# Kernel tuning notes

Measured on AMD Instinct MI355X. Metric: run time of the kernel, lower is better.

## Reference

```python
import jax, jax.numpy as jnp
import numpy as np

B, T, C, H, NUM_EDGE_TYPES = 2, 512, 256, 8, 16


def setup_inputs() -> dict:
    key = jax.random.key(0)
    ks = jax.random.split(key, 8)
    init = 0.02
    x = jax.random.normal(ks[0], (B, T, C), dtype=jnp.float32)
    bias_matrix = jax.random.randint(ks[1], (B, T, T), 0, NUM_EDGE_TYPES)
    w_attn = jax.random.normal(ks[2], (C, 3 * C), dtype=jnp.float32) * init
    w_proj = jax.random.normal(ks[3], (C, C), dtype=jnp.float32) * init
    w_edge_k = jax.random.normal(ks[4], (C, C), dtype=jnp.float32) * init
    w_edge_v = jax.random.normal(ks[5], (C, C), dtype=jnp.float32) * init
    edge_emb_table = jax.random.normal(ks[6], (NUM_EDGE_TYPES, C), dtype=jnp.float32)
    attn_bias_table = jax.random.normal(ks[7], (NUM_EDGE_TYPES, H), dtype=jnp.float32)
    return {
        "x": x,
        "bias_matrix": bias_matrix,
        "w_attn": w_attn,
        "w_proj": w_proj,
        "w_edge_k": w_edge_k,
        "w_edge_v": w_edge_v,
        "edge_emb_table": edge_emb_table,
        "attn_bias_table": attn_bias_table,
    }


def reference(x, bias_matrix, w_attn, w_proj, w_edge_k, w_edge_v,
              edge_emb_table, attn_bias_table):
    b, t, c = x.shape
    h = attn_bias_table.shape[1]
    e = c // h
    scale = jnp.sqrt(jnp.asarray(e, x.dtype))

    qkv = x @ w_attn                              # (B,T,3C)
    q, k, v = jnp.split(qkv, 3, axis=-1)
    # (B,H,T,E)
    q = q.reshape(b, t, h, e).transpose(0, 2, 1, 3)
    k = k.reshape(b, t, h, e).transpose(0, 2, 1, 3)
    v = v.reshape(b, t, h, e).transpose(0, 2, 1, 3)

    # edge-type embeddings and per-pair k/v modulation, (B,T,T,H,E)
    ee = edge_emb_table[bias_matrix]              # (B,T,T,C)
    e_k = (ee @ w_edge_k).reshape(b, t, t, h, e)
    e_v = (ee @ w_edge_v).reshape(b, t, t, h, e)

    # scores[b,h,i,j] = sum_e q[b,h,i,e] * k[b,h,j,e] * e_k[b, j, i, h, e]
    # (torch: e_k permuted to (B,H,j,i,E), broadcast-multiplied by k then
    #  contracted with q via 'bhie,bhjie->bhij')
    scores = jnp.einsum('bhie,bhje,bjihe->bhij', q, k, e_k) / scale

    causal = jnp.tril(jnp.ones((t, t), dtype=bool))  # (T,T)
    scores = jnp.where(causal, scores, -jnp.inf)

    # edge-type attention bias: (B,T,T,H) -> (B,H,T,T), zeroed above diagonal
    bias = attn_bias_table[bias_matrix].transpose(0, 3, 1, 2)
    bias = jnp.where(causal, bias, jnp.zeros((), bias.dtype))

    attn = jax.nn.softmax(scores + bias, axis=-1)  # (B,H,T,T)

    # y[b,h,i,e] = sum_j attn[b,h,i,j] * v[b,h,j,e] * e_v[b, j, i, h, e]
    y = jnp.einsum('bhij,bhje,bjihe->bhie', attn, v, e_v)
    y = y.transpose(0, 2, 1, 3).reshape(b, t, c)
    return y @ w_proj
```

## Files before the change

kernel.cpp:

```cpp
#include <hip/hip_runtime.h>
#include <hip/hip_bf16.h>
#include <math.h>

#define Bdim 2
#define Tdim 512
#define Cdim 256
#define Hdim 8
#define Edim 32
#define NTYPES 16
#define TI 8
#define JT 128

__global__ __launch_bounds__(256) void pre_kernel(
    const float* __restrict__ A, const float* __restrict__ Bw,
    const float* __restrict__ emb, const float* __restrict__ wk,
    const float* __restrict__ wv,
    float* __restrict__ qT, float* __restrict__ kT, float* __restrict__ vT,
    float* __restrict__ ekt, float* __restrict__ evt)
{
    __shared__ float smem[16 * 34 + 16 * 64];
    int tid = threadIdx.x;

    if (blockIdx.x >= 384) {
        int t = blockIdx.x - 384;
        float* se = smem;
        se[tid] = emb[t * Cdim + tid];
        __syncthreads();
        float a = 0.f, b = 0.f;
        for (int k = 0; k < Cdim; ++k) {
            float ev = se[k];
            a = fmaf(ev, wk[k * Cdim + tid], a);
            b = fmaf(ev, wv[k * Cdim + tid], b);
        }
        ekt[t * Cdim + tid] = a;
        evt[t * Cdim + tid] = b;
        return;
    }

    const int N = 3 * Cdim;
    const int K = Cdim;
    float (*As)[34] = (float(*)[34])smem;
    float (*Bs)[64] = (float(*)[64])(smem + 16 * 34);
    int m0 = (blockIdx.x / 12) * 32;
    int n0 = (blockIdx.x % 12) * 64;
    int tr = tid >> 4, tc = tid & 15;
    float acc[2][4] = {};
    int bkr = tid >> 4, bcq = (tid & 15) * 4;

    for (int k0 = 0; k0 < K; k0 += 16) {
        if (tid < 128) {
            int r = tid >> 2, kq = (tid & 3) * 4;
            float4 av = *(const float4*)(A + (size_t)(m0 + r) * K + k0 + kq);
            As[kq + 0][r] = av.x;
            As[kq + 1][r] = av.y;
            As[kq + 2][r] = av.z;
            As[kq + 3][r] = av.w;
        }
        float4 bv = *(const float4*)(Bw + (size_t)(k0 + bkr) * N + n0 + bcq);
        *(float4*)&Bs[bkr][bcq] = bv;
        __syncthreads();
#pragma unroll
        for (int kk = 0; kk < 16; ++kk) {
            float2 a2 = *(float2*)&As[kk][tr * 2];
            float4 b4 = *(float4*)&Bs[kk][tc * 4];
            acc[0][0] = fmaf(a2.x, b4.x, acc[0][0]);
            acc[0][1] = fmaf(a2.x, b4.y, acc[0][1]);
            acc[0][2] = fmaf(a2.x, b4.z, acc[0][2]);
            acc[0][3] = fmaf(a2.x, b4.w, acc[0][3]);
            acc[1][0] = fmaf(a2.y, b4.x, acc[1][0]);
            acc[1][1] = fmaf(a2.y, b4.y, acc[1][1]);
            acc[1][2] = fmaf(a2.y, b4.z, acc[1][2]);
            acc[1][3] = fmaf(a2.y, b4.w, acc[1][3]);
        }
        __syncthreads();
    }
    int sec = n0 >> 8;
    float* dst = (sec == 0) ? qT : (sec == 1) ? kT : vT;
    int cc0 = (n0 & 255) + tc * 4;
    int h = cc0 >> 5;
    int e0 = cc0 & 31;
#pragma unroll
    for (int i = 0; i < 2; ++i) {
        int m = m0 + tr * 2 + i;
        int bq = m >> 9, t = m & (Tdim - 1);
        float4 val = make_float4(acc[i][0], acc[i][1], acc[i][2], acc[i][3]);
        *(float4*)&dst[(((size_t)bq * Hdim + h) * Tdim + t) * Edim + e0] = val;
    }
}

__global__ __launch_bounds__(512, 4) void attn_kernel(
    const float* __restrict__ qT, const float* __restrict__ kT,
    const float* __restrict__ vT, const int* __restrict__ bm,
    const float* __restrict__ ekt, const float* __restrict__ evt,
    const float* __restrict__ abt, float* __restrict__ y)
{
    __shared__ float qm[TI][NTYPES][32];
    __shared__ float ss[TI][512];
    __shared__ unsigned int st1pf[Tdim];
    __shared__ float sevt[NTYPES][36];
    __shared__ float sabt[NTYPES];
    __shared__ float sinv[TI];

    float* spart = (float*)ss;

    const int tau = 63 - (blockIdx.x >> 4);
    const int bh = blockIdx.x & 15;
    const int h = bh & (Hdim - 1);
    const int b = bh >> 3;
    const int tid = threadIdx.x;
    const int wave = tid >> 6;
    const int lane = tid & 63;
    const float inv_scale = 0.17677669529663687f;

    const float* qbase = qT + (size_t)bh * Tdim * Edim;
    const float* kbase = kT + (size_t)bh * Tdim * Edim;
    const float* vbase = vT + (size_t)bh * Tdim * Edim;
    const int* bmb = bm + (size_t)b * Tdim * Tdim;

    const int i0 = tau * TI;
    const int imax = i0 + TI - 1;
    const int njt = (imax >> 7) + 1;
    const int jmax = njt << 7;

    if (tid < 128) {
        int t = tid >> 3, eq = tid & 7;
        *(float4*)&sevt[t][eq * 4] = *(const float4*)&evt[t * Cdim + h * Edim + eq * 4];
    }
    if (tid < NTYPES) sabt[tid] = abt[tid * Hdim + h];
    if (tid < jmax) {
        const int* rowp = bmb + (size_t)tid * Tdim + i0;
        int4 lo = *(const int4*)rowp;
        int4 hi = *(const int4*)(rowp + 4);
        st1pf[tid] =
            ((unsigned)(lo.x & 15)) | (((unsigned)(lo.y & 15)) << 4) |
            (((unsigned)(lo.z & 15)) << 8) | (((unsigned)(lo.w & 15)) << 12) |
            (((unsigned)(hi.x & 15)) << 16) | (((unsigned)(hi.y & 15)) << 20) |
            (((unsigned)(hi.z & 15)) << 24) | (((unsigned)(hi.w & 15)) << 28);
    }
    for (int idx = tid; idx < TI * NTYPES * 8; idx += 512) {
        int eq = idx & 7;
        int t = (idx >> 3) & (NTYPES - 1);
        int r = idx >> 7;
        float4 qv = *(const float4*)&qbase[(size_t)(i0 + r) * Edim + eq * 4];
        float4 ev = *(const float4*)&ekt[t * Cdim + h * Edim + eq * 4];
        float4 o;
        o.x = qv.x * ev.x; o.y = qv.y * ev.y;
        o.z = qv.z * ev.z; o.w = qv.w * ev.w;
        *(float4*)&qm[r][t][(eq << 2) ^ ((t & 7) << 2)] = o;
    }
    __syncthreads();

    {
        const int jsub = wave & 1;
        const int ii0 = wave >> 1;
        const int jl = (jsub << 6) + lane;
        for (int jt = 0; jt < njt; ++jt) {
            int j0 = jt << 7;
            if (j0 + (jsub << 6) > imax) break;
            int j = j0 + jl;
            unsigned tp = st1pf[j];
            const float* krow = kbase + ((size_t)j << 5);
            float4 k4[8];
#pragma unroll
            for (int eq = 0; eq < 8; ++eq)
                k4[eq] = *(const float4*)(krow + eq * 4);

#pragma unroll
            for (int u = 0; u < 2; ++u) {
                int ii = ii0 + (u << 2);
                int i = i0 + ii;
                if (j0 + (jsub << 6) > i) continue;
                int t1 = (tp >> (ii * 4)) & 15;
                const int qsw = (t1 & 7) << 2;
                float s0 = 0.f, s1 = 0.f;
#pragma unroll
                for (int eq = 0; eq < 8; ++eq) {
                    float4 qv = *(float4*)&qm[ii][t1][(eq << 2) ^ qsw];
                    s0 = fmaf(qv.x, k4[eq].x, s0);
                    s1 = fmaf(qv.y, k4[eq].y, s1);
                    s0 = fmaf(qv.z, k4[eq].z, s0);
                    s1 = fmaf(qv.w, k4[eq].w, s1);
                }
                if (j <= i) ss[ii][j] = (s0 + s1) * inv_scale;
            }
        }
    }
    __syncthreads();

    {
        int ii = wave;
        int i = i0 + ii;
        const int* brow = bmb + (size_t)i * Tdim;
        float tb[8];
        float m = -1e30f;
#pragma unroll
        for (int c = 0; c < 8; ++c) {
            int j = (c << 6) + lane;
            float val = ss[ii][j] + sabt[brow[j] & 15];
            tb[c] = (j <= i) ? val : -1e30f;
            m = fmaxf(m, tb[c]);
        }
        for (int off = 32; off; off >>= 1) m = fmaxf(m, __shfl_xor(m, off));
        float sum = 0.f;
#pragma unroll
        for (int c = 0; c < 8; ++c) {
            int j = (c << 6) + lane;
            float p = __expf(tb[c] - m);
            p = (j <= i) ? p : 0.f;
            sum += p;
            if (j <= i) ss[ii][j] = p;
        }
        for (int off = 32; off; off >>= 1) sum += __shfl_xor(sum, off);
        if (lane == 0) sinv[ii] = 1.0f / sum;
    }
    __syncthreads();

    float4 acc[TI];
#pragma unroll
    for (int ii = 0; ii < TI; ++ii) acc[ii] = make_float4(0.f, 0.f, 0.f, 0.f);
    {
        const int gid = tid >> 3;
        const int eqg4 = (tid & 7) << 2;
        for (int jt = 0; jt < njt; ++jt) {
            int j0 = jt << 7;
#pragma unroll
            for (int sub = 0; sub < 2; ++sub) {
                if (j0 + (sub << 6) > imax) continue;
                int jl = (sub << 6) + gid;
                int j = j0 + jl;
                float4 v4 = *(const float4*)&vbase[((size_t)j << 5) + eqg4];
                unsigned tp = st1pf[j];
#pragma unroll
                for (int ii = 0; ii < TI; ++ii) {
                    int i = i0 + ii;
                    if (j0 + (sub << 6) > i) continue;
                    float p = (j <= i) ? ss[ii][j] : 0.f;
                    int t1 = (tp >> (ii * 4)) & 15;
                    float4 ev = *(float4*)&sevt[t1][eqg4];
                    acc[ii].x = fmaf(p * ev.x, v4.x, acc[ii].x);
                    acc[ii].y = fmaf(p * ev.y, v4.y, acc[ii].y);
                    acc[ii].z = fmaf(p * ev.z, v4.z, acc[ii].z);
                    acc[ii].w = fmaf(p * ev.w, v4.w, acc[ii].w);
                }
            }
        }
    }
    __syncthreads();
#pragma unroll
    for (int ii = 0; ii < TI; ++ii) {
#pragma unroll
        for (int m = 8; m <= 32; m <<= 1) {
            acc[ii].x += __shfl_xor(acc[ii].x, m);
            acc[ii].y += __shfl_xor(acc[ii].y, m);
            acc[ii].z += __shfl_xor(acc[ii].z, m);
            acc[ii].w += __shfl_xor(acc[ii].w, m);
        }
    }
    if (lane < 8) {
#pragma unroll
        for (int ii = 0; ii < TI; ++ii)
            *(float4*)&spart[((wave * TI + ii) << 5) + lane * 4] = acc[ii];
    }
    __syncthreads();
    if (tid < TI * Edim) {
        int ii = tid >> 5, e = tid & 31;
        float yv = 0.f;
#pragma unroll
        for (int w = 0; w < 8; ++w) yv += spart[((w * TI + ii) << 5) + e];
        yv *= sinv[ii];
        y[((size_t)(b * Tdim + i0 + ii)) * Cdim + h * Edim + e] = yv;
    }
}

__global__ __launch_bounds__(256) void proj_gemm_kernel(
    const float* __restrict__ A, const float* __restrict__ Bw,
    float* __restrict__ out)
{
    const int N = Cdim;
    const int K = Cdim;
    __shared__ float As[16][34];
    __shared__ float Bs[16][64];
    int m0 = blockIdx.y * 32;
    int n0 = blockIdx.x * 64;
    int tid = threadIdx.x;
    int tr = tid >> 4, tc = tid & 15;
    float acc[2][4] = {};
    int bkr = tid >> 4, bcq = (tid & 15) * 4;

    for (int k0 = 0; k0 < K; k0 += 16) {
        if (tid < 128) {
            int r = tid >> 2, kq = (tid & 3) * 4;
            float4 av = *(const float4*)(A + (size_t)(m0 + r) * K + k0 + kq);
            As[kq + 0][r] = av.x;
            As[kq + 1][r] = av.y;
            As[kq + 2][r] = av.z;
            As[kq + 3][r] = av.w;
        }
        float4 bv = *(const float4*)(Bw + (size_t)(k0 + bkr) * N + n0 + bcq);
        *(float4*)&Bs[bkr][bcq] = bv;
        __syncthreads();
#pragma unroll
        for (int kk = 0; kk < 16; ++kk) {
            float2 a2 = *(float2*)&As[kk][tr * 2];
            float4 b4 = *(float4*)&Bs[kk][tc * 4];
            acc[0][0] = fmaf(a2.x, b4.x, acc[0][0]);
            acc[0][1] = fmaf(a2.x, b4.y, acc[0][1]);
            acc[0][2] = fmaf(a2.x, b4.z, acc[0][2]);
            acc[0][3] = fmaf(a2.x, b4.w, acc[0][3]);
            acc[1][0] = fmaf(a2.y, b4.x, acc[1][0]);
            acc[1][1] = fmaf(a2.y, b4.y, acc[1][1]);
            acc[1][2] = fmaf(a2.y, b4.z, acc[1][2]);
            acc[1][3] = fmaf(a2.y, b4.w, acc[1][3]);
        }
        __syncthreads();
    }
#pragma unroll
    for (int i = 0; i < 2; ++i) {
        int m = m0 + tr * 2 + i;
        float4 val = make_float4(acc[i][0], acc[i][1], acc[i][2], acc[i][3]);
        *(float4*)&out[(size_t)m * N + n0 + tc * 4] = val;
    }
}

extern "C" void kernel_launch(void* const* d_in, const int* in_sizes, int n_in,
                              void* d_out, int out_size, void* d_ws, size_t ws_size,
                              hipStream_t stream) {
    (void)in_sizes; (void)n_in; (void)out_size; (void)ws_size;
    const float* x = (const float*)d_in[0];
    const int* bias_matrix = (const int*)d_in[1];
    const float* w_attn = (const float*)d_in[2];
    const float* w_proj = (const float*)d_in[3];
    const float* w_edge_k = (const float*)d_in[4];
    const float* w_edge_v = (const float*)d_in[5];
    const float* edge_emb = (const float*)d_in[6];
    const float* attn_bias = (const float*)d_in[7];
    float* out = (float*)d_out;

    const size_t n_qkv = (size_t)Bdim * Hdim * Tdim * Edim;
    float* ws = (float*)d_ws;
    float* qT = ws;
    float* kT = qT + n_qkv;
    float* vT = kT + n_qkv;
    float* y = vT + n_qkv;
    float* ekt = y + (size_t)Bdim * Tdim * Cdim;
    float* evt = ekt + (size_t)NTYPES * Cdim;

    pre_kernel<<<400, 256, 0, stream>>>(x, w_attn, edge_emb, w_edge_k, w_edge_v,
                                        qT, kT, vT, ekt, evt);
    attn_kernel<<<dim3(64 * 16), 512, 0, stream>>>(qT, kT, vT, bias_matrix,
                                                   ekt, evt, attn_bias, y);
    proj_gemm_kernel<<<dim3(4, 32), 256, 0, stream>>>(y, w_proj, out);
}
```

Measured before the change: 139.4 us.

## Split score dot products across lane quads with DPP reduction

Restructures the score computation so each group of four lanes shares one key row. Each lane handles an 8-element slice of E for all 8 query rows, and partial sums are combined with DPP quad reductions. The j-range is striped across waves in 16-row chunks, which tightens the causal bound, and the ss rows are padded to reduce LDS bank conflicts. This lowers per-lane register pressure from holding a full 32-float key and evens out work under the causal mask, at the cost of extra DPP ops and some redundant q loads. The PV loop is also flattened into 64-row chunks with no change to the work done.

```diff
diff --git a/kernel.cpp b/kernel.cpp
--- a/kernel.cpp
+++ b/kernel.cpp
@@ -9,7 +9,6 @@
 #define Edim 32
 #define NTYPES 16
 #define TI 8
-#define JT 128
 
 __global__ __launch_bounds__(256) void pre_kernel(
     const float* __restrict__ A, const float* __restrict__ Bw,
@@ -88,6 +87,14 @@
     }
 }
 
+__device__ __forceinline__ float quad_reduce_add(float s) {
+    int t = __builtin_amdgcn_update_dpp(0, __float_as_int(s), 0xB1, 0xF, 0xF, true);
+    s += __int_as_float(t);
+    t = __builtin_amdgcn_update_dpp(0, __float_as_int(s), 0x4E, 0xF, 0xF, true);
+    s += __int_as_float(t);
+    return s;
+}
+
 __global__ __launch_bounds__(512, 4) void attn_kernel(
     const float* __restrict__ qT, const float* __restrict__ kT,
     const float* __restrict__ vT, const int* __restrict__ bm,
@@ -95,7 +102,7 @@
     const float* __restrict__ abt, float* __restrict__ y)
 {
     __shared__ float qm[TI][NTYPES][32];
-    __shared__ float ss[TI][512];
+    __shared__ float ss[TI][516];
     __shared__ unsigned int st1pf[Tdim];
     __shared__ float sevt[NTYPES][36];
     __shared__ float sabt[NTYPES];
@@ -119,8 +126,7 @@
 
     const int i0 = tau * TI;
     const int imax = i0 + TI - 1;
-    const int njt = (imax >> 7) + 1;
-    const int jmax = njt << 7;
+    const int jmax = (((imax >> 7) + 1) << 7);
 
     if (tid < 128) {
         int t = tid >> 3, eq = tid & 7;
@@ -151,38 +157,36 @@
     __syncthreads();
 
     {
-        const int jsub = wave & 1;
-        const int ii0 = wave >> 1;
-        const int jl = (jsub << 6) + lane;
-        for (int jt = 0; jt < njt; ++jt) {
-            int j0 = jt << 7;
-            if (j0 + (jsub << 6) > imax) break;
-            int j = j0 + jl;
+        const int g = lane >> 2;
+        const int c = lane & 3;
+        const int e0 = c << 3;
+        for (int jb = wave << 4; jb <= imax; jb += 128) {
+            const int j = jb + g;
+            const float* krow = kbase + ((size_t)j << 5) + e0;
+            float4 k0 = *(const float4*)(krow);
+            float4 k1 = *(const float4*)(krow + 4);
             unsigned tp = st1pf[j];
-            const float* krow = kbase + ((size_t)j << 5);
-            float4 k4[8];
-#pragma unroll
-            for (int eq = 0; eq < 8; ++eq)
-                k4[eq] = *(const float4*)(krow + eq * 4);
-
-#pragma unroll
-            for (int u = 0; u < 2; ++u) {
-                int ii = ii0 + (u << 2);
-                int i = i0 + ii;
-                if (j0 + (jsub << 6) > i) continue;
+            float my0 = 0.f, my1 = 0.f;
+#pragma unroll
+            for (int ii = 0; ii < 8; ++ii) {
                 int t1 = (tp >> (ii * 4)) & 15;
-                const int qsw = (t1 & 7) << 2;
-                float s0 = 0.f, s1 = 0.f;
-#pragma unroll
-                for (int eq = 0; eq < 8; ++eq) {
-                    float4 qv = *(float4*)&qm[ii][t1][(eq << 2) ^ qsw];
-                    s0 = fmaf(qv.x, k4[eq].x, s0);
-                    s1 = fmaf(qv.y, k4[eq].y, s1);
-                    s0 = fmaf(qv.z, k4[eq].z, s0);
-                    s1 = fmaf(qv.w, k4[eq].w, s1);
-                }
-                if (j <= i) ss[ii][j] = (s0 + s1) * inv_scale;
+                int o0 = e0 ^ ((t1 & 7) << 2);
+                float4 q0 = *(float4*)&qm[ii][t1][o0];
+                float4 q1 = *(float4*)&qm[ii][t1][o0 ^ 4];
+                float s = q0.x * k0.x;
+                s = fmaf(q0.y, k0.y, s);
+                s = fmaf(q0.z, k0.z, s);
+                s = fmaf(q0.w, k0.w, s);
+                s = fmaf(q1.x, k1.x, s);
+                s = fmaf(q1.y, k1.y, s);
+                s = fmaf(q1.z, k1.z, s);
+                s = fmaf(q1.w, k1.w, s);
+                s = quad_reduce_add(s);
+                if (ii < 4) my0 = (c == ii) ? s : my0;
+                else        my1 = (c == (ii - 4)) ? s : my1;
             }
+            if (j <= i0 + c)     ss[c][j]     = my0 * inv_scale;
+            if (j <= i0 + c + 4) ss[c + 4][j] = my1 * inv_scale;
         }
     }
     __syncthreads();
@@ -219,29 +223,23 @@
 #pragma unroll
     for (int ii = 0; ii < TI; ++ii) acc[ii] = make_float4(0.f, 0.f, 0.f, 0.f);
     {
-        const int gid = tid >> 3;
+        const int gid8 = tid >> 3;
         const int eqg4 = (tid & 7) << 2;
-        for (int jt = 0; jt < njt; ++jt) {
-            int j0 = jt << 7;
-#pragma unroll
-            for (int sub = 0; sub < 2; ++sub) {
-                if (j0 + (sub << 6) > imax) continue;
-                int jl = (sub << 6) + gid;
-                int j = j0 + jl;
-                float4 v4 = *(const float4*)&vbase[((size_t)j << 5) + eqg4];
-                unsigned tp = st1pf[j];
-#pragma unroll
-                for (int ii = 0; ii < TI; ++ii) {
-                    int i = i0 + ii;
-                    if (j0 + (sub << 6) > i) continue;
-                    float p = (j <= i) ? ss[ii][j] : 0.f;
-                    int t1 = (tp >> (ii * 4)) & 15;
-                    float4 ev = *(float4*)&sevt[t1][eqg4];
-                    acc[ii].x = fmaf(p * ev.x, v4.x, acc[ii].x);
-                    acc[ii].y = fmaf(p * ev.y, v4.y, acc[ii].y);
-                    acc[ii].z = fmaf(p * ev.z, v4.z, acc[ii].z);
-                    acc[ii].w = fmaf(p * ev.w, v4.w, acc[ii].w);
-                }
+        for (int jc = 0; (jc << 6) <= imax; ++jc) {
+            const int j = (jc << 6) + gid8;
+            float4 v4 = *(const float4*)&vbase[((size_t)j << 5) + eqg4];
+            unsigned tp = st1pf[j];
+#pragma unroll
+            for (int ii = 0; ii < TI; ++ii) {
+                const int i = i0 + ii;
+                if ((jc << 6) > i) continue;
+                float p = (j <= i) ? ss[ii][j] : 0.f;
+                int t1 = (tp >> (ii * 4)) & 15;
+                float4 ev = *(float4*)&sevt[t1][eqg4];
+                acc[ii].x = fmaf(p * ev.x, v4.x, acc[ii].x);
+                acc[ii].y = fmaf(p * ev.y, v4.y, acc[ii].y);
+                acc[ii].z = fmaf(p * ev.z, v4.z, acc[ii].z);
+                acc[ii].w = fmaf(p * ev.w, v4.w, acc[ii].w);
             }
         }
     }
```

Result: faster. 129.0 us (-7.4%).
